# Kernel optimization log

Hardware: AMD Instinct MI355X
Metric: run time of the kernel (lower is better)

Reference implementation:

```python
import jax, jax.numpy as jnp
import numpy as np

EMBED, IN_DIM, HID, LAYERS, NVIEW = 1024, 256, 256, 3, 6


def _lstm_layer(x_seq, Wih, Whh, bih, bhh):
    # x_seq: [BM, N, D]; torch LSTM gate order i,f,g,o
    BM = x_seq.shape[0]
    h0 = jnp.zeros((BM, HID), x_seq.dtype)
    c0 = jnp.zeros((BM, HID), x_seq.dtype)

    def step(carry, x_t):
        h, c = carry
        gates = x_t @ Wih.T + bih + h @ Whh.T + bhh  # [BM, 4H]
        i, f, g, o = jnp.split(gates, 4, axis=-1)
        c = jax.nn.sigmoid(f) * c + jax.nn.sigmoid(i) * jnp.tanh(g)
        h = jax.nn.sigmoid(o) * jnp.tanh(c)
        return (h, c), h

    _, ys = jax.lax.scan(step, (h0, c0), jnp.swapaxes(x_seq, 0, 1))
    return jnp.swapaxes(ys, 0, 1)  # [BM, N, H]


def setup_inputs() -> dict:
    key = jax.random.key(0)
    ks = jax.random.split(key, 16)
    B, M = 32, 256
    s = lambda fan: 1.0 / np.sqrt(fan)
    inp = {
        "b_x_swin": jax.random.normal(ks[0], (B, M, NVIEW, EMBED), jnp.float32),
        "b_x_conv": jax.random.normal(ks[1], (B, M, NVIEW, EMBED), jnp.float32),
        "Wc": jax.random.uniform(ks[2], (EMBED, EMBED), jnp.float32, -s(EMBED), s(EMBED)),
        "bc": jax.random.uniform(ks[3], (EMBED,), jnp.float32, -s(EMBED), s(EMBED)),
        "Win": jax.random.uniform(ks[4], (IN_DIM, EMBED), jnp.float32, -s(EMBED), s(EMBED)),
        "b_in": jax.random.uniform(ks[5], (IN_DIM,), jnp.float32, -s(EMBED), s(EMBED)),
        "Wih": jax.random.uniform(ks[6], (LAYERS, 4 * HID, IN_DIM), jnp.float32, -s(HID), s(HID)),
        "Whh": jax.random.uniform(ks[7], (LAYERS, 4 * HID, HID), jnp.float32, -s(HID), s(HID)),
        "bih": jax.random.uniform(ks[8], (LAYERS, 4 * HID), jnp.float32, -s(HID), s(HID)),
        "bhh": jax.random.uniform(ks[9], (LAYERS, 4 * HID), jnp.float32, -s(HID), s(HID)),
        "Wv": jax.random.uniform(ks[10], (1, HID), jnp.float32, -s(HID), s(HID)),
        "bv": jax.random.uniform(ks[11], (1,), jnp.float32, -s(HID), s(HID)),
        "Ws": jax.random.uniform(ks[12], (1, NVIEW), jnp.float32, -s(NVIEW), s(NVIEW)),
        "bs": jax.random.uniform(ks[13], (1,), jnp.float32, -s(NVIEW), s(NVIEW)),
    }
    return inp


def reference(b_x_swin, b_x_conv, Wc, bc, Win, b_in, Wih, Whh, bih, bhh, Wv, bv, Ws, bs):
    B, M, N, C = b_x_swin.shape
    # fc_conv + exact GELU + residual (vectorized over all samples; same math as per-sample loop)
    x = b_x_swin + jax.nn.gelu(b_x_conv @ Wc.T + bc, approximate=False)
    x = x @ Win.T + b_in                         # [B, M, N, IN_DIM]
    x = x.reshape(B * M, N, IN_DIM)              # LSTM batch = B*M, seq = N
    for l in range(LAYERS):
        x = _lstm_layer(x, Wih[l], Whh[l], bih[l], bhh[l])
    v = (x @ Wv.T + bv).reshape(B, M, N)         # fc_viewport + flatten(1)
    score = (v @ Ws.T + bs).squeeze(-1)          # fc_score -> [B, M]
    return jnp.mean(score, axis=1)               # torch.mean per sample -> [B]
```

## Files before the change

### kernel.cpp

```cpp
#include <hip/hip_runtime.h>
#include <math.h>
#include <stdint.h>

typedef unsigned short u16;
typedef float f32x4 __attribute__((ext_vector_type(4)));
typedef short bf16x8 __attribute__((ext_vector_type(8)));

#define NVIEW 6

__device__ __forceinline__ u16 f2bf(float f){
  unsigned u = __float_as_uint(f);
  u += 0x7FFFu + ((u >> 16) & 1u);
  return (u16)(u >> 16);
}
__device__ __forceinline__ float bf2f(u16 h){
  return __uint_as_float(((unsigned)h) << 16);
}
__device__ __forceinline__ float fsig(float x){
  x = fminf(fmaxf(x, -30.f), 30.f);
  return 1.0f / (1.0f + __expf(-x));
}
__device__ __forceinline__ float ftanh(float x){
  x = fminf(fmaxf(x, -15.f), 15.f);
  float e = __expf(2.0f * x);
  return (e - 1.0f) / (e + 1.0f);
}
__device__ __forceinline__ void gload16(const u16* g, u16* l){
  __builtin_amdgcn_global_load_lds((const __attribute__((address_space(1))) unsigned int*)g,
                                   (__attribute__((address_space(3))) unsigned int*)l,
                                   16, 0, 0);
}

__global__ void k_cvt(const float* __restrict__ in, u16* __restrict__ out, long n4){
  long i = (long)blockIdx.x * blockDim.x + threadIdx.x;
  long stride = (long)gridDim.x * blockDim.x;
  for (; i < n4; i += stride){
    const float4 v = ((const float4*)in)[i];
    ushort4 o;
    o.x = f2bf(v.x); o.y = f2bf(v.y); o.z = f2bf(v.z); o.w = f2bf(v.w);
    ((ushort4*)out)[i] = o;
  }
}

__global__ void k_build_wl(const float* __restrict__ Wih, const float* __restrict__ Whh,
                           u16* __restrict__ Wl){
  int idx = blockIdx.x * 256 + threadIdx.x;
  int l   = idx >> 19;
  int rem = idx & 524287;
  int ro  = rem >> 9;
  int k   = rem & 511;
  int u = ro >> 2, q = ro & 3;
  int ri = q * 256 + u;
  float v = (k < 256) ? Wih[(l * 1024 + ri) * 256 + k]
                      : Whh[(l * 1024 + ri) * 256 + (k - 256)];
  Wl[idx] = f2bf(v);
}

__global__ void k_build_bias(const float* __restrict__ bih, const float* __restrict__ bhh,
                             float* __restrict__ biasL, u16* __restrict__ zbuf){
  int idx = blockIdx.x * 256 + threadIdx.x;
  if (idx < 3072){
    int l = idx >> 10; int ro = idx & 1023;
    int u = ro >> 2, q = ro & 3;
    int ri = q * 256 + u;
    biasL[idx] = bih[l * 1024 + ri] + bhh[l * 1024 + ri];
  }
  if (idx < 256) zbuf[idx] = 0;
}

#define DSR(dst, addr) asm volatile("ds_read_b128 %0, %1" : "=v"(dst) : "v"(addr))

template<int EPI>
__global__ __launch_bounds__(512, 2)
void gemm2p(const u16* __restrict__ A, long sA,
            const u16* __restrict__ Bm, long sB,
            int N, int K,
            const float* __restrict__ bias,
            const float* __restrict__ resid,
            u16* __restrict__ outb)
{
  __shared__ __align__(128) u16 shA[2 * 16384];
  __shared__ __align__(128) u16 shB[2 * 16384];

  const int tid  = threadIdx.x;
  const int lane = tid & 63;
  const int wv   = tid >> 6;
  const int wm   = wv >> 2;
  const int wn   = wv & 3;
  const int wm16 = wm * 16, wn16 = wn * 16;
  const int l15  = lane & 15, lk = lane >> 4;
  const int w2   = wv * 2;

  const int nwg = gridDim.x;
  const int qq  = nwg >> 3;
  const int b   = blockIdx.x;
  const int swz = (b & 7) * qq + (b >> 3);
  const int NB  = N >> 8;
  const long m0 = (long)(swz / NB) * 256;
  const int  n0 = (swz % NB) * 256;

  const int NT = K >> 6;

  const long laneA = (long)(lane >> 3) * sA + (long)(((lane & 7) ^ (lane >> 3)) << 3);
  const long laneB = (long)(lane >> 3) * sB + (long)(((lane & 7) ^ (lane >> 3)) << 3);

  auto STAGE = [&](int buf, int t){
    #pragma unroll
    for (int mh = 0; mh < 2; ++mh)
      #pragma unroll
      for (int j = 0; j < 2; ++j){
        const int chunk = w2 + j;
        gload16(A + (m0 + mh * 128 + chunk * 8) * sA + (long)t * 64 + laneA,
                shA + buf * 16384 + mh * 8192 + chunk * 512 + lane * 8);
      }
    #pragma unroll
    for (int nh = 0; nh < 2; ++nh)
      #pragma unroll
      for (int j = 0; j < 2; ++j){
        const int chunk = w2 + j;
        gload16(Bm + (long)(n0 + nh * 128 + chunk * 8) * sB + (long)t * 64 + laneB,
                shB + buf * 16384 + nh * 8192 + chunk * 512 + lane * 8);
      }
  };

  const unsigned ldsA = (unsigned)(uintptr_t)&shA[0];
  const unsigned ldsB = (unsigned)(uintptr_t)&shB[0];
  const unsigned aA0  = ldsA + (unsigned)((wm16 + l15) * 128 + ((lk ^ (l15 & 7)) << 4));
  const unsigned aB0  = ldsB + (unsigned)((wn16 + l15) * 128 + ((lk ^ (l15 & 7)) << 4));

  f32x4 acc[8][4];
  #pragma unroll
  for (int i = 0; i < 8; ++i)
    #pragma unroll
    for (int j = 0; j < 4; ++j)
      acc[i][j] = (f32x4){0.f, 0.f, 0.f, 0.f};

  STAGE(0, 0);

  for (int t = 0; t < NT; ++t){
    const int cur = t & 1;
    asm volatile("s_waitcnt vmcnt(0)" ::: "memory");
    __builtin_amdgcn_s_barrier();
    if (t + 1 < NT) STAGE(cur ^ 1, t + 1);

    bf16x8 af[2][8], bq[2][4];
    const unsigned bufOff = (unsigned)(cur * 32768);
    const unsigned aA = aA0 + bufOff, aB = aB0 + bufOff;
    #pragma unroll
    for (int mf = 0; mf < 8; ++mf) DSR(af[0][mf], aA + mf * 4096);
    #pragma unroll
    for (int nf = 0; nf < 4; ++nf) DSR(bq[0][nf], aB + nf * 8192);
    #pragma unroll
    for (int mf = 0; mf < 8; ++mf) DSR(af[1][mf], (aA ^ 64) + mf * 4096);
    #pragma unroll
    for (int nf = 0; nf < 4; ++nf) DSR(bq[1][nf], (aB ^ 64) + nf * 8192);

    asm volatile("s_waitcnt lgkmcnt(12)" ::: "memory");
    __builtin_amdgcn_sched_barrier(0);
    __builtin_amdgcn_s_setprio(1);
    #pragma unroll
    for (int mf = 0; mf < 8; ++mf)
      #pragma unroll
      for (int nf = 0; nf < 4; ++nf)
        acc[mf][nf] = __builtin_amdgcn_mfma_f32_16x16x32_bf16(af[0][mf], bq[0][nf], acc[mf][nf], 0, 0, 0);
    __builtin_amdgcn_s_setprio(0);

    asm volatile("s_waitcnt lgkmcnt(0)" ::: "memory");
    __builtin_amdgcn_sched_barrier(0);
    __builtin_amdgcn_s_setprio(1);
    #pragma unroll
    for (int mf = 0; mf < 8; ++mf)
      #pragma unroll
      for (int nf = 0; nf < 4; ++nf)
        acc[mf][nf] = __builtin_amdgcn_mfma_f32_16x16x32_bf16(af[1][mf], bq[1][nf], acc[mf][nf], 0, 0, 0);
    __builtin_amdgcn_s_setprio(0);
  }

  #pragma unroll
  for (int mf = 0; mf < 8; ++mf){
    #pragma unroll
    for (int nf = 0; nf < 4; ++nf){
      const int n = n0 + nf * 64 + wn16 + l15;
      const float bz = bias[n];
      const long mrow = m0 + mf * 32 + wm16 + lk * 4;
      #pragma unroll
      for (int r = 0; r < 4; ++r){
        float v = acc[mf][nf][r] + bz;
        const long off = (mrow + r) * (long)N + n;
        if (EPI == 0){
          float ge = 0.5f * v * (1.0f + erff(v * 0.70710678118654752f));
          v = ge + resid[off];
        }
        outb[off] = f2bf(v);
      }
    }
  }
}

template<int EPI>
__global__ __launch_bounds__(256)
void gemm_bt(const u16* __restrict__ A0, long sA0,
             const u16* __restrict__ A1, long sA1, int K0,
             const u16* __restrict__ Bm,
             int N, int K,
             const float* __restrict__ bias,
             const float* __restrict__ resid,
             u16* __restrict__ outb,
             float* __restrict__ cbuf,
             int tstep)
{
  __shared__ __align__(16) u16 lA[128 * 64];
  __shared__ __align__(16) u16 lB[128 * 64];

  const int tid  = threadIdx.x;
  const int lane = tid & 63;
  const int wid  = tid >> 6;
  const int wm = wid >> 1, wn = wid & 1;
  const int l15 = lane & 15, lk = lane >> 4;
  const long m0 = (long)blockIdx.x * 128;
  const int  n0 = blockIdx.y * 128;

  f32x4 acc[4][4];
  #pragma unroll
  for (int i = 0; i < 4; ++i)
    #pragma unroll
    for (int j = 0; j < 4; ++j)
      acc[i][j] = (f32x4){0.f, 0.f, 0.f, 0.f};

  const int rowL = tid >> 3;
  const int col8 = (tid & 7) * 8;

  for (int kt = 0; kt < (K >> 6); ++kt){
    const int kbase = kt << 6;
    #pragma unroll
    for (int c = 0; c < 4; ++c){
      int r = c * 32 + rowL;
      int k = kbase + col8;
      const u16* src = (k < K0) ? (A0 + (m0 + r) * sA0 + k)
                                : (A1 + (m0 + r) * sA1 + (k - K0));
      gload16(src, &lA[r * 64 + col8]);
    }
    #pragma unroll
    for (int c = 0; c < 4; ++c){
      int r = c * 32 + rowL;
      int k = kbase + col8;
      gload16(Bm + (long)(n0 + r) * K + k, &lB[r * 64 + col8]);
    }
    __syncthreads();

    #pragma unroll
    for (int ks = 0; ks < 2; ++ks){
      bf16x8 af[4], bfr[4];
      #pragma unroll
      for (int mf = 0; mf < 4; ++mf)
        af[mf] = *(const bf16x8*)&lA[(wm * 64 + mf * 16 + l15) * 64 + ks * 32 + lk * 8];
      #pragma unroll
      for (int nf = 0; nf < 4; ++nf)
        bfr[nf] = *(const bf16x8*)&lB[(wn * 64 + nf * 16 + l15) * 64 + ks * 32 + lk * 8];
      #pragma unroll
      for (int mf = 0; mf < 4; ++mf)
        #pragma unroll
        for (int nf = 0; nf < 4; ++nf)
          acc[mf][nf] = __builtin_amdgcn_mfma_f32_16x16x32_bf16(af[mf], bfr[nf], acc[mf][nf], 0, 0, 0);
    }
    __syncthreads();
  }

  if (EPI == 0 || EPI == 1){
    #pragma unroll
    for (int mf = 0; mf < 4; ++mf){
      #pragma unroll
      for (int nf = 0; nf < 4; ++nf){
        int  n    = n0 + wn * 64 + nf * 16 + l15;
        long mrow = m0 + wm * 64 + mf * 16 + lk * 4;
        float bz = bias[n];
        #pragma unroll
        for (int r = 0; r < 4; ++r){
          float v = acc[mf][nf][r] + bz;
          long off = (mrow + r) * N + n;
          if (EPI == 0){
            float ge = 0.5f * v * (1.0f + erff(v * 0.70710678118654752f));
            v = ge + resid[off];
          }
          outb[off] = f2bf(v);
        }
      }
    }
  } else {
    const int a  = lane & 3;
    const int qb = lane & ~3;
    #pragma unroll
    for (int mf = 0; mf < 4; ++mf){
      #pragma unroll
      for (int nf = 0; nf < 4; ++nf){
        int n = n0 + wn * 64 + nf * 16 + l15;
        float bz = bias[n];
        float v0 = acc[mf][nf][0] + bz;
        float v1 = acc[mf][nf][1] + bz;
        float v2 = acc[mf][nf][2] + bz;
        float v3 = acc[mf][nf][3] + bz;
        float s0 = (a == 0) ? v0 : (a == 1) ? v1 : (a == 2) ? v2 : v3;
        float s1 = (a == 0) ? v1 : (a == 1) ? v2 : (a == 2) ? v3 : v0;
        float s2 = (a == 0) ? v2 : (a == 1) ? v3 : (a == 2) ? v0 : v1;
        float s3 = (a == 0) ? v3 : (a == 1) ? v0 : (a == 2) ? v1 : v2;
        float r0 = s0;
        float r1 = __shfl(s1, qb + ((a + 3) & 3));
        float r2 = __shfl(s2, qb + ((a + 2) & 3));
        float r3 = __shfl(s3, qb + ((a + 1) & 3));
        float wi = (a == 0) ? r0 : (a == 1) ? r1 : (a == 2) ? r2 : r3;
        float wf = (a == 1) ? r0 : (a == 2) ? r1 : (a == 3) ? r2 : r3;
        float wg = (a == 2) ? r0 : (a == 3) ? r1 : (a == 0) ? r2 : r3;
        float wo = (a == 3) ? r0 : (a == 0) ? r1 : (a == 1) ? r2 : r3;
        long row = m0 + wm * 64 + mf * 16 + lk * 4 + a;
        int  u   = ((n0 + wn * 64 + nf * 16) >> 2) + (l15 >> 2);
        float c_old = (tstep == 0) ? 0.0f : cbuf[row * 256 + u];
        float ii = fsig(wi), ff = fsig(wf), gg = ftanh(wg), oo = fsig(wo);
        float cn = ff * c_old + ii * gg;
        float hn = oo * ftanh(cn);
        cbuf[row * 256 + u] = cn;
        outb[(row * NVIEW + tstep) * 256 + u] = f2bf(hn);
      }
    }
  }
}

__global__ void k_score(const u16* __restrict__ X3, const float* __restrict__ Wv,
                        const float* __restrict__ bv, const float* __restrict__ Ws,
                        const float* __restrict__ bs, float* __restrict__ score){
  int lane = threadIdx.x & 63;
  int bm = blockIdx.x * 4 + (threadIdx.x >> 6);
  const u16* row = X3 + (long)bm * (NVIEW * 256);
  float4 wv = *(const float4*)(Wv + lane * 4);
  float p = 0.f;
  #pragma unroll
  for (int n = 0; n < NVIEW; ++n){
    ushort4 xv = *(const ushort4*)(row + n * 256 + lane * 4);
    float d = bf2f(xv.x) * wv.x + bf2f(xv.y) * wv.y + bf2f(xv.z) * wv.z + bf2f(xv.w) * wv.w;
    p += Ws[n] * d;
  }
  #pragma unroll
  for (int off = 32; off; off >>= 1) p += __shfl_xor(p, off);
  if (lane == 0){
    float sw = Ws[0] + Ws[1] + Ws[2] + Ws[3] + Ws[4] + Ws[5];
    score[bm] = p + bv[0] * sw + bs[0];
  }
}

__global__ void k_mean(const float* __restrict__ score, float* __restrict__ out){
  __shared__ float red[256];
  int b = blockIdx.x, tid = threadIdx.x;
  red[tid] = score[b * 256 + tid];
  __syncthreads();
  for (int s = 128; s > 0; s >>= 1){
    if (tid < s) red[tid] += red[tid + s];
    __syncthreads();
  }
  if (tid == 0) out[b] = red[0] * (1.0f / 256.0f);
}

extern "C" void kernel_launch(void* const* d_in, const int* in_sizes, int n_in,
                              void* d_out, int out_size, void* d_ws, size_t ws_size,
                              hipStream_t stream){
  const float* swin = (const float*)d_in[0];
  const float* conv = (const float*)d_in[1];
  const float* Wc   = (const float*)d_in[2];
  const float* bc   = (const float*)d_in[3];
  const float* Win  = (const float*)d_in[4];
  const float* b_in = (const float*)d_in[5];
  const float* Wih  = (const float*)d_in[6];
  const float* Whh  = (const float*)d_in[7];
  const float* bih  = (const float*)d_in[8];
  const float* bhh  = (const float*)d_in[9];
  const float* Wv   = (const float*)d_in[10];
  const float* bv   = (const float*)d_in[11];
  const float* Ws   = (const float*)d_in[12];
  const float* bs   = (const float*)d_in[13];
  float* out = (float*)d_out;

  char* w = (char*)d_ws;
  u16*  convb = (u16*)(w);
  u16*  X0    = (u16*)(w);
  u16*  XA    = (u16*)(w + 25165824);
  u16*  XB    = (u16*)(w + 50331648);
  float* cbuf = (float*)(w + 75497472);
  u16*  Y     = (u16*)(w + 100663296);
  u16*  Wcb   = (u16*)(w + 201326592);
  u16*  Winb  = (u16*)(w + 203423744);
  u16*  Wl    = (u16*)(w + 203948032);
  float* biasL= (float*)(w + 207093760);
  u16*  zbuf  = (u16*)(w + 207106048);
  float* scoreb = (float*)(w + 207106560);

  k_cvt<<<4096, 256, 0, stream>>>(conv, convb, 49152L * 1024 / 4);
  k_cvt<<<512, 256, 0, stream>>>(Wc, Wcb, 1048576 / 4);
  k_cvt<<<128, 256, 0, stream>>>(Win, Winb, 262144 / 4);
  k_build_wl<<<6144, 256, 0, stream>>>(Wih, Whh, Wl);
  k_build_bias<<<12, 256, 0, stream>>>(bih, bhh, biasL, zbuf);

  gemm2p<0><<<768, 512, 0, stream>>>(convb, 1024L, Wcb, 1024L,
                                     1024, 1024, bc, swin, Y);

  gemm2p<1><<<192, 512, 0, stream>>>(Y, 1024L, Winb, 1024L,
                                     256, 1024, b_in, (const float*)nullptr, X0);

  const u16* xin = X0;
  u16* xout = XA;
  for (int l = 0; l < 3; ++l){
    for (int t = 0; t < 6; ++t){
      const u16* a1 = (t == 0) ? zbuf : (xout + (t - 1) * 256);
      long s1 = (t == 0) ? 0L : 1536L;
      gemm_bt<2><<<dim3(64, 8), 256, 0, stream>>>(
          xin + t * 256, 1536L, a1, s1, 256,
          Wl + l * 1024 * 512, 1024, 512,
          biasL + l * 1024, (const float*)nullptr,
          xout, cbuf, t);
    }
    if (l == 0){ xin = XA; xout = XB; }
    else if (l == 1){ xin = XB; xout = XA; }
  }

  k_score<<<2048, 256, 0, stream>>>(XA, Wv, bv, Ws, bs, scoreb);
  k_mean<<<32, 256, 0, stream>>>(scoreb, out);
}
```

Baseline: 831.7 us.

## Prepack GEMM operands into tile-contiguous swizzled layout for contiguous LDS staging

The bf16 conversion kernels now write A and B operands in a pre-tiled, pre-swizzled block layout matching the GEMM's LDS tile. Each global_load_lds then reads a contiguous 16KB chunk per stage instead of strided rows. The first GEMM's epilogue writes Y in that same packed layout so the second GEMM can stage it directly. The goal is more coalesced global loads and simpler address arithmetic, at the cost of scattered 2-byte stores in the first GEMM's epilogue.

After: 825.5 us. Within noise of the previous version (-0.8%).

```diff
diff --git a/kernel.cpp b/kernel.cpp
--- a/kernel.cpp
+++ b/kernel.cpp
@@ -5,6 +5,7 @@
 typedef unsigned short u16;
 typedef float f32x4 __attribute__((ext_vector_type(4)));
 typedef short bf16x8 __attribute__((ext_vector_type(8)));
+typedef unsigned short u16x8 __attribute__((ext_vector_type(8)));
 
 #define NVIEW 6
 
@@ -31,14 +32,27 @@
                                    16, 0, 0);
 }
 
-__global__ void k_cvt(const float* __restrict__ in, u16* __restrict__ out, long n4){
-  long i = (long)blockIdx.x * blockDim.x + threadIdx.x;
-  long stride = (long)gridDim.x * blockDim.x;
-  for (; i < n4; i += stride){
-    const float4 v = ((const float4*)in)[i];
-    ushort4 o;
-    o.x = f2bf(v.x); o.y = f2bf(v.y); o.z = f2bf(v.z); o.w = f2bf(v.w);
-    ((ushort4*)out)[i] = o;
+__global__ void k_packA(const float* __restrict__ src, u16* __restrict__ dst,
+                        int Kdim, long noct){
+  const int K8 = Kdim >> 3;
+  const int NT = Kdim >> 6;
+  long g = (long)blockIdx.x * blockDim.x + threadIdx.x;
+  const long stride = (long)gridDim.x * blockDim.x;
+  for (; g < noct; g += stride){
+    const long m  = g / K8;
+    const int  k8 = (int)(g - m * K8);
+    const int  k  = k8 << 3;
+    const float4* p = (const float4*)(src + m * (long)Kdim + k);
+    const float4 v0 = p[0], v1 = p[1];
+    const int mblk = (int)(m >> 8), r = (int)(m & 255);
+    const int kt = k >> 6, c16 = (k >> 3) & 7;
+    const int mh = r >> 7, chunk = (r >> 3) & 15, lnrow = r & 7;
+    const int lane = lnrow * 8 + (c16 ^ lnrow);
+    const long off = (((long)(mblk * NT + kt) * 2 + mh) << 13) + chunk * 512 + lane * 8;
+    u16x8 o;
+    o[0] = f2bf(v0.x); o[1] = f2bf(v0.y); o[2] = f2bf(v0.z); o[3] = f2bf(v0.w);
+    o[4] = f2bf(v1.x); o[5] = f2bf(v1.y); o[6] = f2bf(v1.z); o[7] = f2bf(v1.w);
+    *(u16x8*)(dst + off) = o;
   }
 }
 
@@ -72,8 +86,8 @@
 
 template<int EPI>
 __global__ __launch_bounds__(512, 2)
-void gemm2p(const u16* __restrict__ A, long sA,
-            const u16* __restrict__ Bm, long sB,
+void gemm2p(const u16* __restrict__ A,
+            const u16* __restrict__ Bm,
             int N, int K,
             const float* __restrict__ bias,
             const float* __restrict__ resid,
@@ -96,30 +110,29 @@
   const int b   = blockIdx.x;
   const int swz = (b & 7) * qq + (b >> 3);
   const int NB  = N >> 8;
-  const long m0 = (long)(swz / NB) * 256;
-  const int  n0 = (swz % NB) * 256;
+  const int mblk = swz / NB;
+  const int nblk = swz % NB;
+  const long m0 = (long)mblk * 256;
+  const int  n0 = nblk * 256;
 
   const int NT = K >> 6;
 
-  const long laneA = (long)(lane >> 3) * sA + (long)(((lane & 7) ^ (lane >> 3)) << 3);
-  const long laneB = (long)(lane >> 3) * sB + (long)(((lane & 7) ^ (lane >> 3)) << 3);
-
   auto STAGE = [&](int buf, int t){
+    const u16* baseA = A + (((long)(mblk * NT + t) * 2) << 13);
+    const u16* baseB = Bm + (((long)(nblk * NT + t) * 2) << 13);
     #pragma unroll
     for (int mh = 0; mh < 2; ++mh)
       #pragma unroll
       for (int j = 0; j < 2; ++j){
-        const int chunk = w2 + j;
-        gload16(A + (m0 + mh * 128 + chunk * 8) * sA + (long)t * 64 + laneA,
-                shA + buf * 16384 + mh * 8192 + chunk * 512 + lane * 8);
+        const int off = (mh << 13) + (w2 + j) * 512 + lane * 8;
+        gload16(baseA + off, shA + buf * 16384 + off);
       }
     #pragma unroll
     for (int nh = 0; nh < 2; ++nh)
       #pragma unroll
       for (int j = 0; j < 2; ++j){
-        const int chunk = w2 + j;
-        gload16(Bm + (long)(n0 + nh * 128 + chunk * 8) * sB + (long)t * 64 + laneB,
-                shB + buf * 16384 + nh * 8192 + chunk * 512 + lane * 8);
+        const int off = (nh << 13) + (w2 + j) * 512 + lane * 8;
+        gload16(baseB + off, shB + buf * 16384 + off);
       }
   };
 
@@ -182,16 +195,24 @@
     for (int nf = 0; nf < 4; ++nf){
       const int n = n0 + nf * 64 + wn16 + l15;
       const float bz = bias[n];
-      const long mrow = m0 + mf * 32 + wm16 + lk * 4;
+      const int rloc0 = mf * 32 + wm16 + lk * 4;
       #pragma unroll
       for (int r = 0; r < 4; ++r){
         float v = acc[mf][nf][r] + bz;
-        const long off = (mrow + r) * (long)N + n;
         if (EPI == 0){
+          const long roff = (m0 + rloc0 + r) * (long)N + n;
           float ge = 0.5f * v * (1.0f + erff(v * 0.70710678118654752f));
-          v = ge + resid[off];
+          v = ge + resid[roff];
+          const int rloc = rloc0 + r;
+          const int kt = n >> 6, c16 = (n >> 3) & 7, e = n & 7;
+          const int mh = rloc >> 7, chunk = (rloc >> 3) & 15, lnrow = rloc & 7;
+          const long off = (((long)(mblk * NT  + kt) * 2 + mh) << 13)
+                         + chunk * 512 + (lnrow * 8 + (c16 ^ lnrow)) * 8 + e;
+          outb[off] = f2bf(v);
+        } else {
+          const long off = (m0 + rloc0 + r) * (long)N + n;
+          outb[off] = f2bf(v);
         }
-        outb[off] = f2bf(v);
       }
     }
   }
@@ -378,30 +399,28 @@
   float* out = (float*)d_out;
 
   char* w = (char*)d_ws;
-  u16*  convb = (u16*)(w);
+  u16*  convP = (u16*)(w);
   u16*  X0    = (u16*)(w);
   u16*  XA    = (u16*)(w + 25165824);
   u16*  XB    = (u16*)(w + 50331648);
   float* cbuf = (float*)(w + 75497472);
   u16*  Y     = (u16*)(w + 100663296);
-  u16*  Wcb   = (u16*)(w + 201326592);
-  u16*  Winb  = (u16*)(w + 203423744);
+  u16*  WcP   = (u16*)(w + 201326592);
+  u16*  WinP  = (u16*)(w + 203423744);
   u16*  Wl    = (u16*)(w + 203948032);
   float* biasL= (float*)(w + 207093760);
   u16*  zbuf  = (u16*)(w + 207106048);
   float* scoreb = (float*)(w + 207106560);
 
-  k_cvt<<<4096, 256, 0, stream>>>(conv, convb, 49152L * 1024 / 4);
-  k_cvt<<<512, 256, 0, stream>>>(Wc, Wcb, 1048576 / 4);
-  k_cvt<<<128, 256, 0, stream>>>(Win, Winb, 262144 / 4);
+  k_packA<<<8192, 256, 0, stream>>>(conv, convP, 1024, 49152L * 1024 / 8);
+  k_packA<<<512, 256, 0, stream>>>(Wc, WcP, 1024, 1024L * 1024 / 8);
+  k_packA<<<128, 256, 0, stream>>>(Win, WinP, 1024, 256L * 1024 / 8);
   k_build_wl<<<6144, 256, 0, stream>>>(Wih, Whh, Wl);
   k_build_bias<<<12, 256, 0, stream>>>(bih, bhh, biasL, zbuf);
 
-  gemm2p<0><<<768, 512, 0, stream>>>(convb, 1024L, Wcb, 1024L,
-                                     1024, 1024, bc, swin, Y);
-
-  gemm2p<1><<<192, 512, 0, stream>>>(Y, 1024L, Winb, 1024L,
-                                     256, 1024, b_in, (const float*)nullptr, X0);
+  gemm2p<0><<<768, 512, 0, stream>>>(convP, WcP, 1024, 1024, bc, swin, Y);
+
+  gemm2p<1><<<192, 512, 0, stream>>>(Y, WinP, 256, 1024, b_in, (const float*)nullptr, X0);
 
   const u16* xin = X0;
   u16* xout = XA;
```
